# Kernel tuning notes

Measured on AMD Instinct MI355X. Metric: run time of the kernel, lower is better.

Reference implementation:

```python
import jax, jax.numpy as jnp
import numpy as np

N = 100000      # nodes
E = 1600000     # edges
F_IN = 512      # input features
H = 64          # hidden
R = 2           # relations
B = 30          # bases
NEG_SLOPE = 0.2 # GATConv default


def setup_inputs() -> dict:
    key = jax.random.key(0)
    ks = jax.random.split(key, 14)
    s_in = 1.0 / np.sqrt(F_IN)
    s_h = 1.0 / np.sqrt(H)
    return {
        "x": jax.random.normal(ks[0], (N, F_IN), jnp.float32),
        "edge_index": jax.random.randint(ks[1], (2, E), 0, N),
        "edge_types": jax.random.randint(ks[2], (E,), 0, R),
        # RGCN layer 1 (F_IN -> H), basis-decomposed
        "basis1": jax.random.normal(ks[3], (B, F_IN, H), jnp.float32) * s_in,
        "comp1": jax.random.normal(ks[4], (R, B), jnp.float32) * (1.0 / np.sqrt(B)),
        "root1": jax.random.normal(ks[5], (F_IN, H), jnp.float32) * s_in,
        "bias1": jnp.zeros((H,), jnp.float32),
        # RGCN layer 2 (H -> H)
        "basis2": jax.random.normal(ks[6], (B, H, H), jnp.float32) * s_h,
        "comp2": jax.random.normal(ks[7], (R, B), jnp.float32) * (1.0 / np.sqrt(B)),
        "root2": jax.random.normal(ks[8], (H, H), jnp.float32) * s_h,
        "bias2": jnp.zeros((H,), jnp.float32),
        # GAT (H -> 1, heads=1)
        "gat_w": jax.random.normal(ks[9], (H, 1), jnp.float32) * s_h,
        "att_src": jax.random.normal(ks[10], (1,), jnp.float32),
        "att_dst": jax.random.normal(ks[11], (1,), jnp.float32),
        "gat_bias": jnp.zeros((1,), jnp.float32),
    }


def rgcn_layer(x, src, dst, etype, basis, comp, root, bias):
    # W_r = sum_b comp[r,b] * basis[b]; transform nodes once per relation,
    # then gather per edge (math-equal to PyG's per-edge transform, cheaper).
    W = jnp.einsum('rb,bio->rio', comp, basis)       # [R, in, out]
    h = jnp.einsum('ni,rio->rno', x, W)              # [R, N, out]
    out = x @ root + bias                            # root/self term
    for r in range(R):                               # R=2, fixed small loop
        m = (etype == r).astype(x.dtype)             # [E]
        msg = h[r][src] * m[:, None]                 # gather + mask
        agg = jax.ops.segment_sum(msg, dst, num_segments=N)
        cnt = jax.ops.segment_sum(m, dst, num_segments=N)
        out = out + agg / jnp.maximum(cnt, 1.0)[:, None]   # mean aggr per relation
    return out


def gat_layer(x, src, dst, gat_w, att_src, att_dst, gat_bias):
    # GATConv with heads=1, out=1, add_self_loops=True, negative_slope=0.2
    loop = jnp.arange(N)
    s = jnp.concatenate([src, loop])
    d = jnp.concatenate([dst, loop])
    h = x @ gat_w                                    # [N, 1]
    a_s = h[:, 0] * att_src[0]                       # [N]
    a_d = h[:, 0] * att_dst[0]                       # [N]
    e = jax.nn.leaky_relu(a_s[s] + a_d[d], NEG_SLOPE)  # [E+N]
    emax = jax.ops.segment_max(e, d, num_segments=N)   # every dst has self-loop
    ex = jnp.exp(e - emax[d])
    denom = jax.ops.segment_sum(ex, d, num_segments=N)
    alpha = ex / denom[d]                            # segment softmax over dst
    out = jax.ops.segment_sum(alpha[:, None] * h[s], d, num_segments=N)
    return out + gat_bias


def reference(x, edge_index, edge_types,
              basis1, comp1, root1, bias1,
              basis2, comp2, root2, bias2,
              gat_w, att_src, att_dst, gat_bias):
    src, dst = edge_index[0], edge_index[1]
    x1 = jax.nn.relu(rgcn_layer(x, src, dst, edge_types, basis1, comp1, root1, bias1))
    x2 = rgcn_layer(x1, src, dst, edge_types, basis2, comp2, root2, bias2)
    return gat_layer(x2, src, dst, gat_w, att_src, att_dst, gat_bias)  # [N, 1]
```

## Files before the change

### kernel.cpp

```cpp
#include <hip/hip_runtime.h>
#include <hip/hip_bf16.h>
#include <math.h>

#define NCOL 192
#define BB   30
#define SCAN_T 256
#define SCAN_ELEMS 1024

typedef short bf16x8 __attribute__((ext_vector_type(8)));
typedef float f32x4  __attribute__((ext_vector_type(4)));
typedef unsigned short u16x8 __attribute__((ext_vector_type(8)));

__device__ __forceinline__ ushort f2bf(float f) {
  unsigned u = __float_as_uint(f);
  unsigned r = u + 0x7fff + ((u >> 16) & 1);
  return (ushort)(r >> 16);
}
__device__ __forceinline__ float bf2f(ushort u) {
  return __uint_as_float(((unsigned)u) << 16);
}

__global__ void hist_deg(const int* __restrict__ dst, int* __restrict__ deg, int E) {
  int e = blockIdx.x * blockDim.x + threadIdx.x;
  if (e >= E) return;
  atomicAdd(&deg[dst[e]], 1);
}

__global__ __launch_bounds__(SCAN_T) void scan_local(const int* __restrict__ deg,
                                                     int* __restrict__ rowptr,
                                                     int* __restrict__ partial, int N) {
  __shared__ int sdata[SCAN_T];
  int t = threadIdx.x;
  int base = blockIdx.x * SCAN_ELEMS + t * 4;
  int v[4], s = 0;
#pragma unroll
  for (int k = 0; k < 4; ++k) {
    v[k] = (base + k < N) ? deg[base + k] : 0;
    s += v[k];
  }
  sdata[t] = s;
  __syncthreads();
  for (int off = 1; off < SCAN_T; off <<= 1) {
    int add = (t >= off) ? sdata[t - off] : 0;
    __syncthreads();
    sdata[t] += add;
    __syncthreads();
  }
  int run = sdata[t] - s;
  if (t == SCAN_T - 1) partial[blockIdx.x] = sdata[t];
#pragma unroll
  for (int k = 0; k < 4; ++k) {
    if (base + k <= N) rowptr[base + k] = run;
    run += v[k];
  }
}

__global__ __launch_bounds__(SCAN_T) void scan_partial(int* __restrict__ partial, int nb) {
  __shared__ int sdata[SCAN_T];
  int t = threadIdx.x;
  int v = (t < nb) ? partial[t] : 0;
  sdata[t] = v;
  __syncthreads();
  for (int off = 1; off < SCAN_T; off <<= 1) {
    int add = (t >= off) ? sdata[t - off] : 0;
    __syncthreads();
    sdata[t] += add;
    __syncthreads();
  }
  if (t < nb) partial[t] = sdata[t] - v;
  if (t == nb - 1) partial[nb] = sdata[t];
}

__global__ void scatter_edges(const int* __restrict__ src, const int* __restrict__ dst,
                              const int* __restrict__ et, const int* __restrict__ rowptr,
                              const int* __restrict__ partial,
                              int* __restrict__ fill, int* __restrict__ srcpk, int E) {
  int e = blockIdx.x * blockDim.x + threadIdx.x;
  if (e >= E) return;
  int d = dst[e];
  int pos = rowptr[d] + partial[d >> 10] + atomicAdd(&fill[d], 1);
  srcpk[pos] = src[e] | (et[e] << 30);
}

__device__ __forceinline__ void wpk_one(const float* __restrict__ basis,
                                        const float* __restrict__ comp,
                                        const float* __restrict__ root,
                                        ushort* __restrict__ Wpk, int Kin, int idx) {
  int k = idx / NCOL, j = idx - k * NCOL;
  float v;
  if (j < 64) {
    v = root[k * 64 + j];
  } else {
    int r = (j >> 6) - 1, o = j & 63;
    float s = 0.f;
#pragma unroll
    for (int b = 0; b < BB; ++b)
      s = fmaf(comp[r * BB + b], basis[((size_t)b * Kin + k) * 64 + o], s);
    v = s;
  }
  Wpk[(((size_t)(k >> 3) * NCOL + j) << 3) + (k & 7)] = f2bf(v);
}

__global__ void build_wpk_both(const float* __restrict__ basis1, const float* __restrict__ comp1,
                               const float* __restrict__ root1,
                               const float* __restrict__ basis2, const float* __restrict__ comp2,
                               const float* __restrict__ root2,
                               ushort* __restrict__ Wpk1, ushort* __restrict__ Wpk2) {
  int idx = blockIdx.x * blockDim.x + threadIdx.x;
  if (idx < 512 * NCOL) {
    wpk_one(basis1, comp1, root1, Wpk1, 512, idx);
  } else {
    idx -= 512 * NCOL;
    if (idx < 64 * NCOL) wpk_one(basis2, comp2, root2, Wpk2, 64, idx);
  }
}

template <int K, int BF16IN>
__global__ __launch_bounds__(256, 4) void gemm_mfma(const void* __restrict__ Xv,
                                                    const ushort* __restrict__ Wpk,
                                                    ushort* __restrict__ Y, int N) {
  constexpr int BK  = 64;
  constexpr int NC  = K / BK;
  constexpr int NLD = BF16IN ? (64 * (BK / 8) / 256) : (64 * (BK / 4) / 256);
  __shared__ ushort As[(NC > 1 ? 2 : 1) * 64 * BK];

  const int row0 = blockIdx.x * 64;
  const int tid  = threadIdx.x;
  const int wid  = tid >> 6;
  const int lane = tid & 63;
  const int lrow = lane & 15;
  const int lhi  = lane >> 4;

  const float*  Xf = (const float*)Xv;
  const ushort* Xh = (const ushort*)Xv;

  float4 pfA[BF16IN ? 1 : NLD], pfB[BF16IN ? 1 : NLD];
  u16x8  phA[BF16IN ? NLD : 1], phB[BF16IN ? NLD : 1];

#define LOAD_CHUNK(c, PF, PH)                                                       \
  if constexpr (BF16IN) {                                                           \
    _Pragma("unroll") for (int it = 0; it < NLD; ++it) {                            \
      int idx = tid + it * 256;                                                     \
      int row = idx / (BK / 8), kq = idx - row * (BK / 8);                          \
      int r = row0 + row;                                                           \
      PH[it] = (u16x8){0, 0, 0, 0, 0, 0, 0, 0};                                     \
      if (r < N) PH[it] = ((const u16x8*)Xh)[(size_t)r * (K / 8) + (c) * (BK / 8) + kq]; \
    }                                                                               \
  } else {                                                                          \
    _Pragma("unroll") for (int it = 0; it < NLD; ++it) {                            \
      int idx = tid + it * 256;                                                     \
      int row = idx / (BK / 4), kq = idx - row * (BK / 4);                          \
      int r = row0 + row;                                                           \
      PF[it] = make_float4(0.f, 0.f, 0.f, 0.f);                                     \
      if (r < N) PF[it] = ((const float4*)Xf)[(size_t)r * (K / 4) + (c) * (BK / 4) + kq]; \
    }                                                                               \
  }

#define COMMIT_CHUNK(buf, PF, PH)                                                   \
  {                                                                                 \
    char* Aw = (char*)As + (size_t)(buf) * 64 * BK * 2;                             \
    if constexpr (BF16IN) {                                                         \
      _Pragma("unroll") for (int it = 0; it < NLD; ++it) {                          \
        int idx = tid + it * 256;                                                   \
        int row = idx / (BK / 8), kq = idx - row * (BK / 8);                        \
        int byte = ((row * BK + kq * 8) * 2) ^ ((row & 7) << 4);                    \
        *(u16x8*)(Aw + byte) = PH[it];                                              \
      }                                                                             \
    } else {                                                                        \
      _Pragma("unroll") for (int it = 0; it < NLD; ++it) {                          \
        int idx = tid + it * 256;                                                   \
        int row = idx / (BK / 4), kq = idx - row * (BK / 4);                        \
        ushort4 b;                                                                  \
        b.x = f2bf(PF[it].x); b.y = f2bf(PF[it].y);                                 \
        b.z = f2bf(PF[it].z); b.w = f2bf(PF[it].w);                                 \
        int byte = ((row * BK + kq * 4) * 2) ^ ((row & 7) << 4);                    \
        *(ushort4*)(Aw + byte) = b;                                                 \
      }                                                                             \
    }                                                                               \
  }

  LOAD_CHUNK(0, pfA, phA)
  COMMIT_CHUNK(0, pfA, phA)
  if constexpr (NC > 1) { LOAD_CHUNK(1, pfB, phB) }
  __syncthreads();

  f32x4 acc[4][3];
#pragma unroll
  for (int s = 0; s < 4; ++s)
#pragma unroll
    for (int c = 0; c < 3; ++c) acc[s][c] = (f32x4){0.f, 0.f, 0.f, 0.f};

#pragma unroll
  for (int c = 0; c < NC; ++c) {
    if (c + 2 < NC) {
      if ((c & 1) == 0) { LOAD_CHUNK(c + 2, pfA, phA) }
      else              { LOAD_CHUNK(c + 2, pfB, phB) }
    }
    const char* Ab = (const char*)As + (size_t)(NC > 1 ? (c & 1) : 0) * 64 * BK * 2;
#pragma unroll
    for (int t = 0; t < BK / 32; ++t) {
      int g = (c * (BK / 32) + t) * 4 + lhi;
      const bf16x8* bp = (const bf16x8*)Wpk + (size_t)g * NCOL + wid * 48 + lrow;
      bf16x8 b0 = bp[0];
      bf16x8 b1 = bp[16];
      bf16x8 b2 = bp[32];
      bf16x8 a[4];
#pragma unroll
      for (int s = 0; s < 4; ++s) {
        int arow = s * 16 + lrow;
        int abyte = ((arow * BK + t * 32 + lhi * 8) * 2) ^ ((arow & 7) << 4);
        a[s] = *(const bf16x8*)(Ab + abyte);
      }
#pragma unroll
      for (int s = 0; s < 4; ++s) {
        acc[s][0] = __builtin_amdgcn_mfma_f32_16x16x32_bf16(a[s], b0, acc[s][0], 0, 0, 0);
        acc[s][1] = __builtin_amdgcn_mfma_f32_16x16x32_bf16(a[s], b1, acc[s][1], 0, 0, 0);
        acc[s][2] = __builtin_amdgcn_mfma_f32_16x16x32_bf16(a[s], b2, acc[s][2], 0, 0, 0);
      }
    }
    if (c + 1 < NC) {
      if (((c + 1) & 1) == 0) { COMMIT_CHUNK(0, pfA, phA) }
      else                    { COMMIT_CHUNK(1, pfB, phB) }
      __syncthreads();
    }
  }
#undef LOAD_CHUNK
#undef COMMIT_CHUNK

#pragma unroll
  for (int s = 0; s < 4; ++s) {
#pragma unroll
    for (int cc = 0; cc < 3; ++cc) {
#pragma unroll
      for (int j = 0; j < 4; ++j) {
        int r = row0 + s * 16 + lhi * 4 + j;
        if (r < N) Y[(size_t)r * NCOL + wid * 48 + cc * 16 + lrow] = f2bf(acc[s][cc][j]);
      }
    }
  }
}

template <int RELU, int GATH>
__global__ __launch_bounds__(256) void fused_agg(const ushort* __restrict__ Y,
                                                 const int* __restrict__ rowptr,
                                                 const int* __restrict__ partial,
                                                 const int* __restrict__ srcpk,
                                                 const float* __restrict__ bias,
                                                 const float* __restrict__ gw,
                                                 ushort* __restrict__ accout,
                                                 float* __restrict__ hval, int N) {
  int n = blockIdx.x * 4 + (threadIdx.x >> 6);
  if (n >= N) return;
  const int lane = threadIdx.x & 63;
  const int g    = lane >> 3;
  const int f0   = (lane & 7) * 8;

  float a0[8], a1[8];
#pragma unroll
  for (int j = 0; j < 8; ++j) { a0[j] = 0.f; a1[j] = 0.f; }
  float c0 = 0.f, c1 = 0.f;

  const int beg = rowptr[n] + partial[n >> 10];
  const int end = rowptr[n + 1] + partial[(n + 1) >> 10];
  for (int i = beg; i < end; i += 16) {
    int eA = i + g, eB = i + 8 + g;
    bool vA = eA < end, vB = eB < end;
    int pkA = 0, pkB = 0;
    if (vA) pkA = srcpk[eA];
    if (vB) pkB = srcpk[eB];
    u16x8 xA = (u16x8){0, 0, 0, 0, 0, 0, 0, 0}, xB = xA;
    if (vA) xA = *(const u16x8*)(Y + (size_t)(pkA & 0x3fffffff) * NCOL + 64 +
                                 ((pkA >> 30) << 6) + f0);
    if (vB) xB = *(const u16x8*)(Y + (size_t)(pkB & 0x3fffffff) * NCOL + 64 +
                                 ((pkB >> 30) << 6) + f0);
    float rA = (vA && (pkA >> 30)) ? 1.f : 0.f;
    float sA = vA ? 1.f : 0.f;
    float rB = (vB && (pkB >> 30)) ? 1.f : 0.f;
    float sB = vB ? 1.f : 0.f;
    c0 += (sA - rA) + (sB - rB);
    c1 += rA + rB;
#pragma unroll
    for (int j = 0; j < 8; ++j) {
      float fA = bf2f(xA[j]), fB = bf2f(xB[j]);
      a0[j] += (sA - rA) * fA + (sB - rB) * fB;
      a1[j] += rA * fA + rB * fB;
    }
  }

#pragma unroll
  for (int msk = 8; msk <= 32; msk <<= 1) {
#pragma unroll
    for (int j = 0; j < 8; ++j) {
      a0[j] += __shfl_xor(a0[j], msk);
      a1[j] += __shfl_xor(a1[j], msk);
    }
    c0 += __shfl_xor(c0, msk);
    c1 += __shfl_xor(c1, msk);
  }

  float inv0 = 1.f / fmaxf(c0, 1.f);
  float inv1 = 1.f / fmaxf(c1, 1.f);
  u16x8 rv = *(const u16x8*)(Y + (size_t)n * NCOL + f0);
  float4 bA = *(const float4*)(bias + f0);
  float4 bB = *(const float4*)(bias + f0 + 4);
  float bb[8] = {bA.x, bA.y, bA.z, bA.w, bB.x, bB.y, bB.z, bB.w};
  float res[8];
#pragma unroll
  for (int j = 0; j < 8; ++j) {
    float v = bf2f(rv[j]) + bb[j] + a0[j] * inv0 + a1[j] * inv1;
    res[j] = RELU ? fmaxf(v, 0.f) : v;
  }
  if (accout && g == 0) {
    u16x8 o;
#pragma unroll
    for (int j = 0; j < 8; ++j) o[j] = f2bf(res[j]);
    *(u16x8*)(accout + (size_t)n * 64 + f0) = o;
  }
  if (GATH) {
    float4 gA = *(const float4*)(gw + f0);
    float4 gB = *(const float4*)(gw + f0 + 4);
    float gg[8] = {gA.x, gA.y, gA.z, gA.w, gB.x, gB.y, gB.z, gB.w};
    float dot = 0.f;
#pragma unroll
    for (int j = 0; j < 8; ++j) dot = fmaf(res[j], gg[j], dot);
    dot += __shfl_xor(dot, 1);
    dot += __shfl_xor(dot, 2);
    dot += __shfl_xor(dot, 4);
    if (lane == 0) hval[n] = dot;
  }
}

__device__ __forceinline__ float leaky(float x) { return x > 0.f ? x : 0.2f * x; }

__global__ __launch_bounds__(256) void gat_csr(const int* __restrict__ rowptr,
                                               const int* __restrict__ partial,
                                               const int* __restrict__ srcpk,
                                               const float* __restrict__ hval,
                                               const float* __restrict__ as_,
                                               const float* __restrict__ ad_,
                                               const float* __restrict__ gb,
                                               float* __restrict__ out, int N) {
  int n = blockIdx.x * 4 + (threadIdx.x >> 6);
  if (n >= N) return;
  const int lane = threadIdx.x & 63;
  float as = *as_, ad = *ad_;
  float hv = hval[n];
  float adn = hv * ad;
  float eself = leaky(hv * as + adn);
  const int beg = rowptr[n] + partial[n >> 10];
  const int end = rowptr[n + 1] + partial[(n + 1) >> 10];
  int deg = end - beg;
  float m, den, acc;
  if (deg <= 64) {
    bool valid = lane < deg;
    float hs = 0.f;
    if (valid) hs = hval[srcpk[beg + lane] & 0x3fffffff];
    float e = valid ? leaky(hs * as + adn) : -3.4e38f;
    m = fmaxf(e, eself);
#pragma unroll
    for (int o = 32; o > 0; o >>= 1) m = fmaxf(m, __shfl_xor(m, o));
    float ex = valid ? expf(e - m) : 0.f;
    den = ex;
    acc = ex * hs;
#pragma unroll
    for (int o = 32; o > 0; o >>= 1) {
      den += __shfl_xor(den, o);
      acc += __shfl_xor(acc, o);
    }
  } else {
    m = eself;
    for (int i = beg + lane; i < end; i += 64)
      m = fmaxf(m, leaky(hval[srcpk[i] & 0x3fffffff] * as + adn));
#pragma unroll
    for (int o = 32; o > 0; o >>= 1) m = fmaxf(m, __shfl_xor(m, o));
    float dl = 0.f, al = 0.f;
    for (int i = beg + lane; i < end; i += 64) {
      float hs = hval[srcpk[i] & 0x3fffffff];
      float ex = expf(leaky(hs * as + adn) - m);
      dl += ex;
      al += ex * hs;
    }
    den = dl;
    acc = al;
#pragma unroll
    for (int o = 32; o > 0; o >>= 1) {
      den += __shfl_xor(den, o);
      acc += __shfl_xor(acc, o);
    }
  }
  float es = expf(eself - m);
  den += es;
  acc += es * hv;
  if (lane == 0) out[n] = acc / den + *gb;
}

extern "C" void kernel_launch(void* const* d_in, const int* in_sizes, int n_in,
                              void* d_out, int out_size, void* d_ws, size_t ws_size,
                              hipStream_t stream) {
  const float* x      = (const float*)d_in[0];
  const int*   eidx   = (const int*)d_in[1];
  const int*   etype  = (const int*)d_in[2];
  const float* basis1 = (const float*)d_in[3];
  const float* comp1  = (const float*)d_in[4];
  const float* root1  = (const float*)d_in[5];
  const float* bias1  = (const float*)d_in[6];
  const float* basis2 = (const float*)d_in[7];
  const float* comp2  = (const float*)d_in[8];
  const float* root2  = (const float*)d_in[9];
  const float* bias2  = (const float*)d_in[10];
  const float* gat_w  = (const float*)d_in[11];
  const float* att_s  = (const float*)d_in[12];
  const float* att_d  = (const float*)d_in[13];
  const float* gat_b  = (const float*)d_in[14];

  const int N = in_sizes[0] / 512;
  const int E = in_sizes[1] / 2;
  const int* src = eidx;
  const int* dst = eidx + E;

  char* p = (char*)d_ws;
  ushort* Y    = (ushort*)p; p += (size_t)N * NCOL * 2;
  ushort* acc1 = (ushort*)p; p += (size_t)N * 64 * 2;
  ushort* Wpk1 = (ushort*)p; p += (size_t)512 * NCOL * 2;
  ushort* Wpk2 = (ushort*)p; p += (size_t)64 * NCOL * 2;
  float* hval  = (float*)p;  p += (size_t)N * 4;
  int* deg     = (int*)p;    p += (size_t)N * 4;
  int* fill    = (int*)p;    p += (size_t)N * 4;
  int* rowptr  = (int*)p;    p += (size_t)(N + 16) * 4;
  int* partial = (int*)p;    p += (size_t)(SCAN_T + 16) * 4;
  int* srcpk   = (int*)p;    p += (size_t)E * 4;
  float* out   = (float*)d_out;

  const int TB = 256;
  const int GB = (N + 63) / 64;
  const int nb = (N + 1 + SCAN_ELEMS - 1) / SCAN_ELEMS;

  hipMemsetAsync(deg, 0, (size_t)2 * N * sizeof(int), stream);
  hist_deg<<<(E + TB - 1) / TB, TB, 0, stream>>>(dst, deg, E);
  scan_local<<<nb, SCAN_T, 0, stream>>>(deg, rowptr, partial, N);
  scan_partial<<<1, SCAN_T, 0, stream>>>(partial, nb);
  scatter_edges<<<(E + TB - 1) / TB, TB, 0, stream>>>(src, dst, etype, rowptr, partial,
                                                      fill, srcpk, E);

  build_wpk_both<<<(576 * NCOL + TB - 1) / TB, TB, 0, stream>>>(basis1, comp1, root1,
                                                                basis2, comp2, root2,
                                                                Wpk1, Wpk2);

  gemm_mfma<512, 0><<<GB, 256, 0, stream>>>(x, Wpk1, Y, N);
  fused_agg<1, 0><<<(N + 3) / 4, TB, 0, stream>>>(Y, rowptr, partial, srcpk, bias1, nullptr,
                                                  acc1, nullptr, N);

  gemm_mfma<64, 1><<<GB, 256, 0, stream>>>(acc1, Wpk2, Y, N);
  fused_agg<0, 1><<<(N + 3) / 4, TB, 0, stream>>>(Y, rowptr, partial, srcpk, bias2, gat_w,
                                                  nullptr, hval, N);

  gat_csr<<<(N + 3) / 4, TB, 0, stream>>>(rowptr, partial, srcpk, hval, att_s, att_d, gat_b,
                                          out, N);
}
```

Before: 420.7 us.

## Give each wave its own 16-row A tile and drop block barriers in GEMM

The MFMA GEMM now has each wave own 16 rows and all 192 output columns, with a private LDS slice for its A rows. Before, the four waves split the columns and shared a 64-row A tile. Because each wave only reads LDS it wrote itself, the __syncthreads barriers are removed. The cost is that every wave now loads all of the packed W columns, four times more B traffic per block from L1/L2, and A reuse across waves is lost. A wave still reads its own LDS writes with no barrier or explicit wait, so correctness depends on compiler or hardware ordering of LDS accesses within a wave.

```diff
diff --git a/kernel.cpp b/kernel.cpp
--- a/kernel.cpp
+++ b/kernel.cpp
@@ -121,15 +121,17 @@
                                                     ushort* __restrict__ Y, int N) {
   constexpr int BK  = 64;
   constexpr int NC  = K / BK;
-  constexpr int NLD = BF16IN ? (64 * (BK / 8) / 256) : (64 * (BK / 4) / 256);
-  __shared__ ushort As[(NC > 1 ? 2 : 1) * 64 * BK];
-
-  const int row0 = blockIdx.x * 64;
+  constexpr int NB  = (NC > 1) ? 2 : 1;
+  constexpr int NLD = BF16IN ? 2 : 4;
+  __shared__ ushort As[4 * NB * 16 * BK];
+
   const int tid  = threadIdx.x;
   const int wid  = tid >> 6;
   const int lane = tid & 63;
   const int lrow = lane & 15;
   const int lhi  = lane >> 4;
+  const int row0 = blockIdx.x * 64 + wid * 16;
+  ushort* myL = As + wid * (NB * 16 * BK);
 
   const float*  Xf = (const float*)Xv;
   const ushort* Xh = (const ushort*)Xv;
@@ -137,58 +139,55 @@
   float4 pfA[BF16IN ? 1 : NLD], pfB[BF16IN ? 1 : NLD];
   u16x8  phA[BF16IN ? NLD : 1], phB[BF16IN ? NLD : 1];
 
-#define LOAD_CHUNK(c, PF, PH)                                                       \
-  if constexpr (BF16IN) {                                                           \
-    _Pragma("unroll") for (int it = 0; it < NLD; ++it) {                            \
-      int idx = tid + it * 256;                                                     \
-      int row = idx / (BK / 8), kq = idx - row * (BK / 8);                          \
-      int r = row0 + row;                                                           \
-      PH[it] = (u16x8){0, 0, 0, 0, 0, 0, 0, 0};                                     \
+#define LOAD_CHUNK(c, PF, PH)                                                        \
+  if constexpr (BF16IN) {                                                            \
+    _Pragma("unroll") for (int it = 0; it < NLD; ++it) {                             \
+      int idx = it * 64 + lane;                                                      \
+      int row = idx >> 3, kq = idx & 7;                                              \
+      int r = row0 + row;                                                            \
+      PH[it] = (u16x8){0, 0, 0, 0, 0, 0, 0, 0};                                      \
       if (r < N) PH[it] = ((const u16x8*)Xh)[(size_t)r * (K / 8) + (c) * (BK / 8) + kq]; \
-    }                                                                               \
-  } else {                                                                          \
-    _Pragma("unroll") for (int it = 0; it < NLD; ++it) {                            \
-      int idx = tid + it * 256;                                                     \
-      int row = idx / (BK / 4), kq = idx - row * (BK / 4);                          \
-      int r = row0 + row;                                                           \
-      PF[it] = make_float4(0.f, 0.f, 0.f, 0.f);                                     \
+    }                                                                                \
+  } else {                                                                           \
+    _Pragma("unroll") for (int it = 0; it < NLD; ++it) {                             \
+      int idx = it * 64 + lane;                                                      \
+      int row = idx >> 4, kq = idx & 15;                                             \
+      int r = row0 + row;                                                            \
+      PF[it] = make_float4(0.f, 0.f, 0.f, 0.f);                                      \
       if (r < N) PF[it] = ((const float4*)Xf)[(size_t)r * (K / 4) + (c) * (BK / 4) + kq]; \
-    }                                                                               \
-  }
-
-#define COMMIT_CHUNK(buf, PF, PH)                                                   \
-  {                                                                                 \
-    char* Aw = (char*)As + (size_t)(buf) * 64 * BK * 2;                             \
-    if constexpr (BF16IN) {                                                         \
-      _Pragma("unroll") for (int it = 0; it < NLD; ++it) {                          \
-        int idx = tid + it * 256;                                                   \
-        int row = idx / (BK / 8), kq = idx - row * (BK / 8);                        \
-        int byte = ((row * BK + kq * 8) * 2) ^ ((row & 7) << 4);                    \
-        *(u16x8*)(Aw + byte) = PH[it];                                              \
-      }                                                                             \
-    } else {                                                                        \
-      _Pragma("unroll") for (int it = 0; it < NLD; ++it) {                          \
-        int idx = tid + it * 256;                                                   \
-        int row = idx / (BK / 4), kq = idx - row * (BK / 4);                        \
-        ushort4 b;                                                                  \
-        b.x = f2bf(PF[it].x); b.y = f2bf(PF[it].y);                                 \
-        b.z = f2bf(PF[it].z); b.w = f2bf(PF[it].w);                                 \
-        int byte = ((row * BK + kq * 4) * 2) ^ ((row & 7) << 4);                    \
-        *(ushort4*)(Aw + byte) = b;                                                 \
-      }                                                                             \
-    }                                                                               \
+    }                                                                                \
+  }
+
+#define COMMIT_CHUNK(buf, PF, PH)                                                    \
+  {                                                                                  \
+    char* Aw = (char*)myL + (size_t)(buf) * 16 * BK * 2;                             \
+    if constexpr (BF16IN) {                                                          \
+      _Pragma("unroll") for (int it = 0; it < NLD; ++it) {                           \
+        int idx = it * 64 + lane;                                                    \
+        int row = idx >> 3, kq = idx & 7;                                            \
+        int byte = ((row * BK + kq * 8) * 2) ^ ((row & 7) << 4);                     \
+        *(u16x8*)(Aw + byte) = PH[it];                                               \
+      }                                                                              \
+    } else {                                                                         \
+      _Pragma("unroll") for (int it = 0; it < NLD; ++it) {                           \
+        int idx = it * 64 + lane;                                                    \
+        int row = idx >> 4, kq = idx & 15;                                           \
+        ushort4 b;                                                                   \
+        b.x = f2bf(PF[it].x); b.y = f2bf(PF[it].y);                                  \
+        b.z = f2bf(PF[it].z); b.w = f2bf(PF[it].w);                                  \
+        int byte = ((row * BK + kq * 4) * 2) ^ ((row & 7) << 4);                     \
+        *(ushort4*)(Aw + byte) = b;                                                  \
+      }                                                                              \
+    }                                                                                \
   }
 
   LOAD_CHUNK(0, pfA, phA)
   COMMIT_CHUNK(0, pfA, phA)
   if constexpr (NC > 1) { LOAD_CHUNK(1, pfB, phB) }
-  __syncthreads();
-
-  f32x4 acc[4][3];
-#pragma unroll
-  for (int s = 0; s < 4; ++s)
-#pragma unroll
-    for (int c = 0; c < 3; ++c) acc[s][c] = (f32x4){0.f, 0.f, 0.f, 0.f};
+
+  f32x4 acc[12];
+#pragma unroll
+  for (int cc = 0; cc < 12; ++cc) acc[cc] = (f32x4){0.f, 0.f, 0.f, 0.f};
 
 #pragma unroll
   for (int c = 0; c < NC; ++c) {
@@ -196,46 +195,38 @@
       if ((c & 1) == 0) { LOAD_CHUNK(c + 2, pfA, phA) }
       else              { LOAD_CHUNK(c + 2, pfB, phB) }
     }
-    const char* Ab = (const char*)As + (size_t)(NC > 1 ? (c & 1) : 0) * 64 * BK * 2;
+    const char* Ab = (const char*)myL + (size_t)(NB > 1 ? (c & 1) : 0) * 16 * BK * 2;
 #pragma unroll
     for (int t = 0; t < BK / 32; ++t) {
+      int abyte = ((lrow * BK + t * 32 + lhi * 8) * 2) ^ ((lrow & 7) << 4);
+      bf16x8 a = *(const bf16x8*)(Ab + abyte);
       int g = (c * (BK / 32) + t) * 4 + lhi;
-      const bf16x8* bp = (const bf16x8*)Wpk + (size_t)g * NCOL + wid * 48 + lrow;
-      bf16x8 b0 = bp[0];
-      bf16x8 b1 = bp[16];
-      bf16x8 b2 = bp[32];
-      bf16x8 a[4];
-#pragma unroll
-      for (int s = 0; s < 4; ++s) {
-        int arow = s * 16 + lrow;
-        int abyte = ((arow * BK + t * 32 + lhi * 8) * 2) ^ ((arow & 7) << 4);
-        a[s] = *(const bf16x8*)(Ab + abyte);
-      }
-#pragma unroll
-      for (int s = 0; s < 4; ++s) {
-        acc[s][0] = __builtin_amdgcn_mfma_f32_16x16x32_bf16(a[s], b0, acc[s][0], 0, 0, 0);
-        acc[s][1] = __builtin_amdgcn_mfma_f32_16x16x32_bf16(a[s], b1, acc[s][1], 0, 0, 0);
-        acc[s][2] = __builtin_amdgcn_mfma_f32_16x16x32_bf16(a[s], b2, acc[s][2], 0, 0, 0);
+      const bf16x8* bp = (const bf16x8*)Wpk + (size_t)g * NCOL + lrow;
+#pragma unroll
+      for (int h = 0; h < 2; ++h) {
+        bf16x8 b[6];
+#pragma unroll
+        for (int q = 0; q < 6; ++q) b[q] = bp[(h * 6 + q) * 16];
+#pragma unroll
+        for (int q = 0; q < 6; ++q)
+          acc[h * 6 + q] = __builtin_amdgcn_mfma_f32_16x16x32_bf16(a, b[q],
+                                                                   acc[h * 6 + q], 0, 0, 0);
       }
     }
     if (c + 1 < NC) {
       if (((c + 1) & 1) == 0) { COMMIT_CHUNK(0, pfA, phA) }
       else                    { COMMIT_CHUNK(1, pfB, phB) }
-      __syncthreads();
     }
   }
 #undef LOAD_CHUNK
 #undef COMMIT_CHUNK
 
 #pragma unroll
-  for (int s = 0; s < 4; ++s) {
-#pragma unroll
-    for (int cc = 0; cc < 3; ++cc) {
-#pragma unroll
-      for (int j = 0; j < 4; ++j) {
-        int r = row0 + s * 16 + lhi * 4 + j;
-        if (r < N) Y[(size_t)r * NCOL + wid * 48 + cc * 16 + lrow] = f2bf(acc[s][cc][j]);
-      }
+  for (int cc = 0; cc < 12; ++cc) {
+#pragma unroll
+    for (int j = 0; j < 4; ++j) {
+      int r = row0 + lhi * 4 + j;
+      if (r < N) Y[(size_t)r * NCOL + cc * 16 + lrow] = f2bf(acc[cc][j]);
     }
   }
 }
```

New measurement: 442.3 us. +5.1%, slower.
